# Kernel optimization log

Hardware: AMD Instinct MI355X
Metric: run time of the kernel (lower is better)

## Reference

```python
import jax, jax.numpy as jnp
import numpy as np

NUM_ANCHORS = 32
MAX_DIST = 3
DDE_ROUNDS = 2
DDE_REV_ROUNDS = 2
PE_ANCHOR_DIM = 16


def setup_inputs() -> dict:
    key = jax.random.key(0)
    ks = jax.random.split(key, 20)
    N, Ntext, NT, E, R, D, H = 20000, 19500, 500, 200000, 500, 256, 256
    PE = DDE_ROUNDS + DDE_REV_ROUNDS + PE_ANCHOR_DIM + 3
    s = 0.02
    return {
        "h_ids": jax.random.randint(ks[0], (E,), 0, N),
        "r_ids": jax.random.randint(ks[1], (E,), 0, R),
        "t_ids": jax.random.randint(ks[2], (E,), 0, N),
        "q_emb": jax.random.normal(ks[3], (D,), jnp.float32),
        "entity_embs": jax.random.normal(ks[4], (Ntext, D), jnp.float32),
        "relation_embs": jax.random.normal(ks[5], (R, D), jnp.float32),
        "topic_entity_ids": jax.random.randint(ks[6], (4,), 0, N),
        "num_entities": N,
        "num_non_text_entities": NT,
        "non_text_emb": jax.random.normal(ks[7], (1, D)) * s,
        "dist_emb": jax.random.normal(ks[8], (MAX_DIST + 2, PE_ANCHOR_DIM)) * s,
        "W_enc": jax.random.normal(ks[9], (D + PE, H)) * s,
        "b_enc": jnp.zeros((H,)),
        "gnn_W_msg": jax.random.normal(ks[10], (2, H + D, H)) * s,
        "gnn_W_gate": jax.random.normal(ks[11], (2, 2 * H, H)) * s,
        "gnn_W_upd": jax.random.normal(ks[12], (2, H, H)) * s,
        "W_out": jax.random.normal(ks[13], (H, D)) * s,
        "scorer_W1": jax.random.normal(ks[14], (4 * D + 4, H)) * s,
        "scorer_b1": jnp.zeros((H,)),
        "scorer_W2": jax.random.normal(ks[15], (H, 1)) * s,
        "scorer_b2": jnp.zeros((1,)),
    }


def reference(h_ids, r_ids, t_ids, q_emb, entity_embs, relation_embs,
              topic_entity_ids, num_entities, num_non_text_entities,
              non_text_emb, dist_emb, W_enc, b_enc,
              gnn_W_msg, gnn_W_gate, gnn_W_upd, W_out,
              scorer_W1, scorer_b1, scorer_W2, scorer_b2):
    N = num_entities
    D = q_emb.shape[0]
    E = h_ids.shape[0]
    # assemble all entity embeddings (text + broadcast non-text)
    all_emb = jnp.concatenate(
        [entity_embs, jnp.broadcast_to(non_text_emb, (num_non_text_entities, D))], axis=0)
    # anchor triple selection: question-conditioned triple scores, top-k
    qe = all_emb @ q_emb            # [N]
    qr = relation_embs @ q_emb      # [R]
    tri_score = qe[h_ids] + qr[r_ids] + qe[t_ids]  # [E]
    anchor_scores, anchor_idx = jax.lax.top_k(tri_score, NUM_ANCHORS)
    # topic DDE positional encoding (mean-aggregated label propagation)
    topic = jnp.zeros((N,), all_emb.dtype).at[topic_entity_ids].set(1.0)
    deg_t = jnp.maximum(jnp.zeros((N,)).at[t_ids].add(1.0), 1.0)
    deg_h = jnp.maximum(jnp.zeros((N,)).at[h_ids].add(1.0), 1.0)
    cols = []
    s = topic
    for _ in range(DDE_ROUNDS):
        s = jnp.zeros((N,)).at[t_ids].add(s[h_ids]) / deg_t
        cols.append(s)
    s = topic
    for _ in range(DDE_REV_ROUNDS):
        s = jnp.zeros((N,)).at[h_ids].add(s[t_ids]) / deg_h
        cols.append(s)
    pe_topic = jnp.stack(cols, axis=1)  # [N, 4]
    # anchor proximity PE: bounded BFS distance, embedded
    anchor_mask = (jnp.zeros((N,)).at[h_ids[anchor_idx]].set(1.0)
                   .at[t_ids[anchor_idx]].set(1.0))
    FAR = float(MAX_DIST + 1)
    dist = jnp.where(anchor_mask > 0, 0.0, FAR)
    for _ in range(MAX_DIST):
        c1 = jnp.full((N,), FAR).at[t_ids].min(dist[h_ids] + 1.0)
        c2 = jnp.full((N,), FAR).at[h_ids].min(dist[t_ids] + 1.0)
        dist = jnp.minimum(dist, jnp.minimum(c1, c2))
    pe_anchor = dist_emb[dist.astype(jnp.int32)]  # [N, 16]
    # path indicators (topic flag, anchor-endpoint flag, subgraph mask = full graph)
    path_ind = jnp.stack([topic, anchor_mask, jnp.ones((N,))], axis=1)
    pe_full = jnp.concatenate([pe_topic, pe_anchor, path_ind], axis=1)  # [N, 23]
    # gated GNN refine over the (full) anchor subgraph
    h = jax.nn.relu(jnp.concatenate([all_emb, pe_full], axis=1) @ W_enc + b_enc)
    rel_e = relation_embs[r_ids]  # [E, D]
    for l in range(gnn_W_msg.shape[0]):
        msg = jax.nn.relu(jnp.concatenate([h[h_ids], rel_e], axis=1) @ gnn_W_msg[l])
        agg = jnp.zeros_like(h).at[t_ids].add(msg)
        gate = jax.nn.sigmoid(jnp.concatenate([h, agg], axis=1) @ gnn_W_gate[l])
        h = h + gate * jnp.tanh(agg @ gnn_W_upd[l])
    h_final = h @ W_out  # back to emb_dim, assembled over all entities
    # scalar triple features
    is_anchor = jnp.zeros((E,)).at[anchor_idx].set(1.0)
    a_score = jnp.zeros((E,)).at[anchor_idx].set(jax.lax.stop_gradient(anchor_scores))
    scalar_feats = jnp.stack([is_anchor, a_score, topic[h_ids], topic[t_ids]], axis=1)
    # triple scorer MLP
    feats = jnp.concatenate([
        jnp.broadcast_to(q_emb, (E, D)), h_final[h_ids], rel_e,
        h_final[t_ids], scalar_feats], axis=1)  # [E, 4D+4]
    hid = jax.nn.relu(feats @ scorer_W1 + scorer_b1)
    return (hid @ scorer_W2 + scorer_b2)[:, 0]
```

## Files before the change

### kernel.cpp

```cpp
#include <hip/hip_runtime.h>
#include <math.h>

#define CDIV(a,b) (((a)+(b)-1)/(b))

typedef short short8 __attribute__((ext_vector_type(8)));
typedef float f32x4  __attribute__((ext_vector_type(4)));
typedef unsigned short u16;

__device__ __forceinline__ float warp_sum(float v){
  #pragma unroll
  for (int o=32;o;o>>=1) v += __shfl_down(v,o);
  return v;
}
__device__ __forceinline__ int warp_min(int v){
  #pragma unroll
  for (int o=32;o;o>>=1) v = min(v,__shfl_down(v,o));
  return v;
}
__device__ __forceinline__ u16 f2bf(float f){
  unsigned u = __float_as_uint(f);
  unsigned r = 0x7fffu + ((u>>16)&1u);
  return (u16)((u + r)>>16);
}
__device__ __forceinline__ float bl(u16 v){ return __uint_as_float(((unsigned)v)<<16); }

__global__ __launch_bounds__(256)
void k_rowdot_all(const float* __restrict__ ent, const float* __restrict__ nontext,
                  const float* __restrict__ q, float* __restrict__ qe,
                  int N, int Ntext,
                  const float* __restrict__ rel, float* __restrict__ qr, int R, int nb1){
  int wid = threadIdx.x>>6, lane = threadIdx.x&63;
  const float* src; float* dst; int row;
  if ((int)blockIdx.x < nb1){
    row = blockIdx.x*4 + wid; if (row >= N) return;
    src = (row < Ntext) ? (ent + (size_t)row*256) : nontext;
    dst = qe;
  } else {
    row = (blockIdx.x-nb1)*4 + wid; if (row >= R) return;
    src = rel + (size_t)row*256;
    dst = qr;
  }
  float4 a = *(const float4*)(src + lane*4);
  float4 b = *(const float4*)(q + lane*4);
  float s = a.x*b.x + a.y*b.y + a.z*b.z + a.w*b.w;
  s = warp_sum(s);
  if (!lane) dst[row] = s;
}

__global__ __launch_bounds__(256)
void k_tri(const int* __restrict__ h, const int* __restrict__ r,
           const int* __restrict__ t, const float* __restrict__ qe,
           const float* __restrict__ qr, float* __restrict__ tri,
           float* __restrict__ bmax, int* __restrict__ degh, int* __restrict__ degi, int E){
  __shared__ float red[256];
  int e = blockIdx.x*256 + threadIdx.x;
  float v = -INFINITY;
  if (e < E){
    int hh=h[e], rr=r[e], tt=t[e];
    v = qe[hh] + qr[rr] + qe[tt];
    tri[e] = v;
    atomicAdd(&degh[hh], 1);
    atomicAdd(&degi[tt], 1);
  }
  red[threadIdx.x]=v; __syncthreads();
  for (int s=128;s;s>>=1){ if ((int)threadIdx.x<s) red[threadIdx.x]=fmaxf(red[threadIdx.x],red[threadIdx.x+s]); __syncthreads(); }
  if (!threadIdx.x) bmax[blockIdx.x]=red[0];
}

__global__ __launch_bounds__(64)
void k_thresh(const float* __restrict__ bmax, float* __restrict__ thrT, int nb){
  int lane = threadIdx.x;
  float m = -INFINITY;
  for (int i=lane; i<nb; i+=64) m = fmaxf(m, bmax[i]);
  for (int it=0; it<32; it++){
    float bv = m; int bln = lane;
    #pragma unroll
    for (int o=32;o;o>>=1){
      float ov = __shfl_down(bv,o);
      int   ol = __shfl_down(bln,o);
      if (ov>bv){ bv=ov; bln=ol; }
    }
    float mv = __shfl(bv,0);
    int   wl = __shfl(bln,0);
    if (lane==wl) m = -INFINITY;
    if (it==31 && lane==0) thrT[0]=mv;
  }
}

__global__ void k_compact(const float* __restrict__ tri, const float* __restrict__ thrT,
                          int* __restrict__ cnt, int* __restrict__ ci, float* __restrict__ cv, int E){
  int e = blockIdx.x*256 + threadIdx.x; if (e>=E) return;
  float v = tri[e];
  if (v >= thrT[0]){
    int p = atomicAdd(cnt, 1);
    ci[p]=e; cv[p]=v;
  }
}

__global__ __launch_bounds__(64)
void k_final32(const int* __restrict__ ci, const float* __restrict__ cv, const int* __restrict__ cnt,
               int* __restrict__ ai, float* __restrict__ as,
               const int* __restrict__ h_ids, const int* __restrict__ t_ids,
               const int* __restrict__ topicId, int nTopic,
               float* __restrict__ topic, float* __restrict__ amask){
  int lane = threadIdx.x;
  int C = *cnt; if (C > 1024) C = 1024;
  int nIter = CDIV(C,64);
  unsigned selMask = 0;
  int myai=0; float myas=0.f;
  for (int it=0; it<32; it++){
    float bv=-INFINITY; int bi=0x7fffffff; int bj=-1;
    for (int j=0;j<nIter;j++){
      int p = lane + j*64;
      if (p < C && !((selMask>>j)&1u)){
        float v = cv[p]; int idx = ci[p];
        if (v>bv || (v==bv && idx<bi)){ bv=v; bi=idx; bj=j; }
      }
    }
    int bln = lane;
    #pragma unroll
    for (int o=32;o;o>>=1){
      float ov=__shfl_down(bv,o); int oi=__shfl_down(bi,o);
      int   oj=__shfl_down(bj,o); int ol=__shfl_down(bln,o);
      if (ov>bv || (ov==bv && oi<bi)){ bv=ov; bi=oi; bj=oj; bln=ol; }
    }
    float wv=__shfl(bv,0); int wi=__shfl(bi,0);
    int   wj=__shfl(bj,0); int wl=__shfl(bln,0);
    if (lane==wl) selMask |= (1u<<wj);
    if (lane==it){ myai=wi; myas=wv; }
  }
  if (lane<32){
    ai[lane]=myai; as[lane]=myas;
    int e = myai;
    amask[h_ids[e]]=1.f;
    amask[t_ids[e]]=1.f;
  }
  if (lane<nTopic) topic[topicId[lane]]=1.f;
}

__global__ void k_scan1(const int* __restrict__ degT, const int* __restrict__ degH,
                        int* __restrict__ offsT, int* __restrict__ offsH,
                        int* __restrict__ bsum, int N, int nb){
  __shared__ int s[256];
  int which = (int)blockIdx.x >= nb;
  int b = which ? blockIdx.x - nb : blockIdx.x;
  const int* deg = which ? degH : degT;
  int* offs = which ? offsH : offsT;
  int i = b*256 + threadIdx.x;
  int v = (i<N) ? deg[i] : 0;
  s[threadIdx.x] = v; __syncthreads();
  #pragma unroll
  for (int o=1;o<256;o<<=1){
    int add = (threadIdx.x>=(unsigned)o) ? s[threadIdx.x-o] : 0; __syncthreads();
    s[threadIdx.x] += add; __syncthreads();
  }
  if (i<N) offs[i] = s[threadIdx.x] - v;
  if (threadIdx.x==255) bsum[blockIdx.x] = s[255];
}
__global__ void k_scan2two(int* __restrict__ bsum, int nb){
  __shared__ int s[256];
  int t=threadIdx.x;
  int half = t>>7, idx = t&127;
  int v = (idx<nb)? bsum[half*nb+idx] : 0;
  s[t]=v; __syncthreads();
  #pragma unroll
  for (int o=1;o<128;o<<=1){ int add=(idx>=o)?s[t-o]:0; __syncthreads(); s[t]+=add; __syncthreads(); }
  if (idx<nb) bsum[half*nb+idx] = s[t]-v;
}
__global__ void k_scan3(int* __restrict__ offsT, int* __restrict__ offsH,
                        const int* __restrict__ bsum,
                        int* __restrict__ curT, int* __restrict__ curH, int N, int nb){
  int which = (int)blockIdx.x >= nb;
  int b = which ? blockIdx.x - nb : blockIdx.x;
  int i = b*256+threadIdx.x; if (i>=N) return;
  int* offs = which ? offsH : offsT;
  int* cur  = which ? curH  : curT;
  int o = offs[i] + bsum[blockIdx.x];
  offs[i]=o; cur[i]=o;
}
__global__ void k_place(const int* __restrict__ h, const int* __restrict__ r,
                        const int* __restrict__ t,
                        int* __restrict__ curT, int* __restrict__ curH,
                        int2* __restrict__ ehr, int* __restrict__ eIdx,
                        int* __restrict__ etH, int E){
  int e = blockIdx.x*256+threadIdx.x; if (e>=E) return;
  int hh=h[e], tt=t[e];
  int pos = atomicAdd(&curT[tt], 1);
  ehr[pos] = make_int2(hh, r[e]);
  eIdx[pos] = e;
  int posh = atomicAdd(&curH[hh], 1);
  etH[posh] = tt;
}

__global__ __launch_bounds__(256)
void k_dde2(const int* __restrict__ offsT, const int* __restrict__ degT, const int2* __restrict__ ehr,
            const int* __restrict__ offsH, const int* __restrict__ degH, const int* __restrict__ etH,
            const float* __restrict__ s0, const float* __restrict__ s1,
            float* __restrict__ sn0, float* __restrict__ sn1,
            float* __restrict__ pe4, int c0, int c1,
            const float* __restrict__ amask, int* __restrict__ dist0, int N){
  int wid=threadIdx.x>>6, lane=threadIdx.x&63;
  int i = blockIdx.x*4+wid; if (i>=N) return;
  int dir = blockIdx.y;
  const int* offs = dir ? offsH : offsT;
  const int* deg  = dir ? degH  : degT;
  const float* s  = dir ? s1 : s0;
  float* sn       = dir ? sn1 : sn0;
  int col         = dir ? c1 : c0;
  int start=offs[i], cnt=deg[i];
  float a=0.f;
  if (dir){
    for (int k=lane;k<cnt;k+=64) a += s[etH[start+k]];
  } else {
    for (int k=lane;k<cnt;k+=64) a += s[ehr[start+k].x];
  }
  a = warp_sum(a);
  if (!lane){
    float v = a / fmaxf((float)cnt,1.f);
    if (sn) sn[i]=v;
    pe4[i*4+col]=v;
    if (dist0 && !dir) dist0[i] = (amask[i]>0.f)?0:4;
  }
}

__global__ __launch_bounds__(256)
void k_bfs_g(const int* __restrict__ offsT, const int* __restrict__ degT, const int2* __restrict__ ehr,
             const int* __restrict__ offsH, const int* __restrict__ degH, const int* __restrict__ etH,
             const int* __restrict__ din, int* __restrict__ dout, int N){
  int wid=threadIdx.x>>6, lane=threadIdx.x&63;
  int i = blockIdx.x*4+wid; if (i>=N) return;
  int sT=offsT[i], cT=degT[i];
  int sH=offsH[i], cH=degH[i];
  int best = 4;
  for (int k=lane;k<cT;k+=64) best = min(best, din[ehr[sT+k].x]+1);
  for (int k=lane;k<cH;k+=64) best = min(best, din[etH[sH+k]]+1);
  best = warp_min(best);
  if (!lane) dout[i] = min(din[i], best);
}

__global__ void k_smalls(const float* __restrict__ dist_e, const float* __restrict__ W_enc,
                         float* __restrict__ distW,
                         const float* __restrict__ nontext, float* __restrict__ encnt,
                         const float* __restrict__ q, const float* __restrict__ W1,
                         const float* __restrict__ b1, float* __restrict__ bias2){
  int b = blockIdx.x, j = threadIdx.x;
  if (b < 5){
    const float* Wpe = W_enc + (256+4)*256;
    float s=0.f;
    #pragma unroll
    for (int p=0;p<16;p++) s += dist_e[b*16+p]*Wpe[p*256+j];
    distW[b*256+j]=s;
  } else if (b == 5){
    float s=0.f;
    for (int k=0;k<256;k++) s += nontext[k]*W_enc[k*256+j];
    encnt[j]=s;
  } else {
    float s=b1[j];
    for (int k=0;k<256;k++) s += q[k]*W1[k*256+j];
    bias2[j]=s;
  }
}

__global__ __launch_bounds__(64)
void k_packall(const float* __restrict__ W_enc, const float* __restrict__ W_msg,
               const float* __restrict__ W_gate, const float* __restrict__ W_upd,
               const float* __restrict__ W1, u16* __restrict__ pbAll){
  int f = blockIdx.x, lane = threadIdx.x;
  int tgt, fid, nt16;
  if      (f < 128) { tgt=0; fid=f;      nt16=16; }
  else if (f < 256) { tgt=1; fid=f-128;  nt16=16; }
  else if (f < 384) { tgt=2; fid=f-256;  nt16=16; }
  else if (f < 896) { tgt=3; fid=f-384;  nt16=32; }
  else if (f < 1408){ tgt=4; fid=f-896;  nt16=32; }
  else if (f < 1792){ tgt=5; fid=f-1408; nt16=48; }
  else              { tgt=6; fid=f-1792; nt16=32; }
  int ks = fid/nt16, nt = fid%nt16;
  int kb = ks*32 + 8*(lane>>4);
  int n  = nt*16 + (lane&15);
  u16 v[8];
  #pragma unroll
  for (int i=0;i<8;i++){
    int k = kb+i;
    float x;
    if (tgt==0) x = W_enc[(size_t)k*256+n];
    else if (tgt==1) x = W_msg[(size_t)k*256+n];
    else if (tgt==2) x = W_msg[(size_t)(512+k)*256+n];
    else if (tgt==3 || tgt==4){
      const float* Wg = W_gate + (tgt==4 ? (size_t)512*256 : 0);
      const float* Wu = W_upd  + (tgt==4 ? (size_t)256*256 : 0);
      int blk = n>>4, c = ((blk>>1)<<4) | (n&15);
      if ((blk&1)==0) x = Wg[(size_t)k*256+c];
      else            x = (k<256) ? 0.f : Wu[(size_t)(k-256)*256+c];
    }
    else if (tgt==5){
      if (n<256)      x = W_msg[(size_t)(256+k)*256+n];
      else if (n<512) x = W_msg[(size_t)(768+k)*256+(n-256)];
      else            x = W1[(size_t)(512+k)*256+(n-512)];
    } else {
      if (n<256) x = W1[(size_t)(256+k)*256+n];
      else       x = W1[(size_t)(768+k)*256+(n-256)];
    }
    v[i]=f2bf(x);
  }
  *(uint4*)(pbAll + ((size_t)f*64+lane)*8) = *(uint4*)v;
}

__global__ __launch_bounds__(64)
void k_packf32(const float* __restrict__ W, u16* __restrict__ Bp){
  int f = blockIdx.x, lane = threadIdx.x;
  int ks = f/32, nt = f%32;
  int kb = ks*32 + 8*(lane>>4);
  int n  = nt*16 + (lane&15);
  u16 v[8];
  #pragma unroll
  for (int i=0;i<8;i++) v[i] = f2bf(W[(size_t)(kb+i)*512 + n]);
  *(uint4*)(Bp + ((size_t)f*64+lane)*8) = *(uint4*)v;
}

template<int NCOLS, int CT, int MODE, bool AF32, int MR>
__global__ __launch_bounds__(256)
void k_bgemm(const float* __restrict__ A1f, const u16* __restrict__ A2a,
             const u16* __restrict__ A2b, int K1,
             const u16* __restrict__ Bp, void* __restrict__ Cout,
             const float* __restrict__ xb, const float* __restrict__ W_enc,
             const float* __restrict__ pe4, const int* __restrict__ dist,
             const float* __restrict__ topic, const float* __restrict__ amask,
             const float* __restrict__ distW,
             int M, int K)
{
  constexpr int NT16 = NCOLS/16;
  constexpr int CPB  = NCOLS/CT;
  constexpr int NREP = CPB/32;
  const int tid  = threadIdx.x;
  const int lane = tid & 63;
  const int w    = tid >> 6;
  const int wr   = w >> 1, wc = w & 1;
  const int ct   = blockIdx.y;
  const int row0 = (blockIdx.x*2 + wr)*(16*MR);
  const int lrow = lane & 15;
  const int kc   = lane >> 4;
  int arow[MR];
  #pragma unroll
  for (int m=0;m<MR;m++){
    int rr = row0 + m*16 + lrow;
    arow[m] = (rr >= M) ? M-1 : rr;
  }

  f32x4 acc[MR][NREP];
  #pragma unroll
  for (int m=0;m<MR;m++)
    #pragma unroll
    for (int n=0;n<NREP;n++) acc[m][n] = (f32x4){0.f,0.f,0.f,0.f};

  const int ksteps = K/32;
  const int fcolBase = ct*(CPB/16) + wc*NREP;

  auto do_step = [&](short8* af, int ks){
    const u16* bp = Bp + ((size_t)(ks*NT16 + fcolBase)*64 + lane)*8;
    #pragma unroll
    for (int n=0;n<NREP;n++){
      short8 bf = *(const short8*)(bp + (size_t)n*64*8);
      #pragma unroll
      for (int m=0;m<MR;m++)
        acc[m][n] = __builtin_amdgcn_mfma_f32_16x16x32_bf16(af[m], bf, acc[m][n], 0, 0, 0);
    }
  };

  if (AF32){
    for (int ks=0; ks<ksteps; ks++){
      short8 af[MR];
      #pragma unroll
      for (int m=0;m<MR;m++){
        const float* ap = A1f + (size_t)arow[m]*256 + ks*32 + kc*8;
        float4 a0 = *(const float4*)ap;
        float4 a1 = *(const float4*)(ap+4);
        af[m][0]=(short)f2bf(a0.x); af[m][1]=(short)f2bf(a0.y); af[m][2]=(short)f2bf(a0.z); af[m][3]=(short)f2bf(a0.w);
        af[m][4]=(short)f2bf(a1.x); af[m][5]=(short)f2bf(a1.y); af[m][6]=(short)f2bf(a1.z); af[m][7]=(short)f2bf(a1.w);
      }
      do_step(af, ks);
    }
  } else {
    int s1 = K1>>5; if (s1 > ksteps) s1 = ksteps;
    for (int ks=0; ks<s1; ks++){
      short8 af[MR];
      #pragma unroll
      for (int m=0;m<MR;m++)
        af[m] = *(const short8*)(A2a + (size_t)arow[m]*256 + ks*32 + kc*8);
      do_step(af, ks);
    }
    for (int ks=s1; ks<ksteps; ks++){
      short8 af[MR];
      #pragma unroll
      for (int m=0;m<MR;m++)
        af[m] = *(const short8*)(A2b + (size_t)arow[m]*256 + (ks-s1)*32 + kc*8);
      do_step(af, ks);
    }
  }

  #pragma unroll
  for (int m=0;m<MR;m++){
    #pragma unroll
    for (int r=0;r<4;r++){
      int orow = row0 + m*16 + 4*kc + r;
      if (orow >= M) continue;
      if (MODE==0 || MODE==1){
        #pragma unroll
        for (int n=0;n<NREP;n++){
          int col = ct*CPB + wc*(CPB/2) + n*16 + lrow;
          float v = acc[m][n][r];
          if (MODE==0) ((float*)Cout)[(size_t)orow*NCOLS + col] = v;
          else         ((u16*)Cout)[(size_t)orow*NCOLS + col] = f2bf(v);
        }
      } else if (MODE==5){
        float tp = topic[orow];
        #pragma unroll
        for (int n=0;n<NREP;n++){
          int col = ct*CPB + wc*(CPB/2) + n*16 + lrow;
          float v = acc[m][n][r] + tp*xb[col];
          ((u16*)Cout)[(size_t)orow*NCOLS + col] = f2bf(v);
        }
      } else if (MODE==6){
        #pragma unroll
        for (int n=0;n<NREP;n++){
          int col = ct*CPB + wc*(CPB/2) + n*16 + lrow;
          float v = acc[m][n][r];
          if (col >= 512) v += xb[col-512];
          ((u16*)Cout)[(size_t)orow*NCOLS + col] = f2bf(v);
        }
      } else if (MODE==3){
        float p0=pe4[orow*4+0], p1=pe4[orow*4+1], p2=pe4[orow*4+2], p3=pe4[orow*4+3];
        int dd=dist[orow];
        float tp=topic[orow], am=amask[orow];
        const float* Wpe = W_enc + 256*256;
        #pragma unroll
        for (int n=0;n<NREP;n++){
          int col = ct*CPB + wc*(CPB/2) + n*16 + lrow;
          float v = acc[m][n][r];
          v += xb[col] + Wpe[22*256+col]
             + p0*Wpe[col] + p1*Wpe[256+col] + p2*Wpe[512+col] + p3*Wpe[768+col]
             + distW[dd*256+col] + tp*Wpe[20*256+col] + am*Wpe[21*256+col];
          ((u16*)Cout)[(size_t)orow*256 + col] = f2bf(fmaxf(v, 0.f));
        }
      } else {
        #pragma unroll
        for (int k=0;k<NREP/2;k++){
          int col = (ct*(CPB/32) + wc*(CPB/64) + k)*16 + lrow;
          size_t idx = (size_t)orow*256 + col;
          float g = 1.f/(1.f+expf(-acc[m][2*k][r]));
          float u = tanhf(acc[m][2*k+1][r]);
          float v = bl(A2a[idx]) + g*u;
          ((u16*)Cout)[idx] = f2bf(v);
        }
      }
    }
  }
}

__global__ __launch_bounds__(256)
void k_encnt_fill(const float* __restrict__ encnt, const float* __restrict__ b_enc,
                  const float* __restrict__ W_enc, const float* __restrict__ pe4,
                  const int* __restrict__ dist, const float* __restrict__ topic,
                  const float* __restrict__ amask, const float* __restrict__ distW,
                  u16* __restrict__ hB, int Ntext){
  int i = Ntext + blockIdx.x, j = threadIdx.x;
  const float* Wpe = W_enc + 256*256;
  float p0=pe4[i*4+0], p1=pe4[i*4+1], p2=pe4[i*4+2], p3=pe4[i*4+3];
  int d = dist[i];
  float tp = topic[i], am = amask[i];
  float v = encnt[j] + b_enc[j] + Wpe[22*256+j]
          + p0*Wpe[j] + p1*Wpe[256+j] + p2*Wpe[512+j] + p3*Wpe[768+j]
          + distW[d*256+j] + tp*Wpe[20*256+j] + am*Wpe[21*256+j];
  hB[(size_t)i*256+j] = f2bf(fmaxf(v, 0.f));
}

__global__ __launch_bounds__(256)
void k_agg(const int* __restrict__ offs, const int* __restrict__ degi,
           const int2* __restrict__ ehr,
           const u16* __restrict__ hm, const u16* __restrict__ relC, int colOff,
           u16* __restrict__ agg, int N){
  int wid = threadIdx.x>>6, lane = threadIdx.x&63;
  int i = blockIdx.x*4 + wid; if (i>=N) return;
  int start = offs[i], cnt = degi[i];
  int c4 = lane*4;
  float a0=0.f,a1=0.f,a2=0.f,a3=0.f;
  int k=0;
  for (; k+3<cnt; k+=4){
    int2 hr[4]; uint2 ua[4], ub[4];
    #pragma unroll
    for (int j=0;j<4;j++) hr[j] = ehr[start+k+j];
    #pragma unroll
    for (int j=0;j<4;j++){
      ua[j] = *(const uint2*)(hm + (size_t)hr[j].x*256 + c4);
      ub[j] = *(const uint2*)(relC + (size_t)hr[j].y*768 + colOff + c4);
    }
    #pragma unroll
    for (int j=0;j<4;j++){
      a0 += fmaxf(bl((u16)(ua[j].x&0xffff))+bl((u16)(ub[j].x&0xffff)),0.f);
      a1 += fmaxf(bl((u16)(ua[j].x>>16))  +bl((u16)(ub[j].x>>16)),  0.f);
      a2 += fmaxf(bl((u16)(ua[j].y&0xffff))+bl((u16)(ub[j].y&0xffff)),0.f);
      a3 += fmaxf(bl((u16)(ua[j].y>>16))  +bl((u16)(ub[j].y>>16)),  0.f);
    }
  }
  for (; k<cnt; k++){
    int2 hr = ehr[start+k];
    uint2 ua = *(const uint2*)(hm + (size_t)hr.x*256 + c4);
    uint2 ub = *(const uint2*)(relC + (size_t)hr.y*768 + colOff + c4);
    a0 += fmaxf(bl((u16)(ua.x&0xffff))+bl((u16)(ub.x&0xffff)),0.f);
    a1 += fmaxf(bl((u16)(ua.x>>16))  +bl((u16)(ub.x>>16)),  0.f);
    a2 += fmaxf(bl((u16)(ua.y&0xffff))+bl((u16)(ub.y&0xffff)),0.f);
    a3 += fmaxf(bl((u16)(ua.y>>16))  +bl((u16)(ub.y>>16)),  0.f);
  }
  uint2 o;
  o.x = (unsigned)f2bf(a0) | ((unsigned)f2bf(a1)<<16);
  o.y = (unsigned)f2bf(a2) | ((unsigned)f2bf(a3)<<16);
  *(uint2*)(agg + (size_t)i*256 + c4) = o;
}

__global__ __launch_bounds__(256)
void k_score(const int* __restrict__ offs, const int* __restrict__ degi,
             const int2* __restrict__ ehr, const int* __restrict__ eIdx,
             const u16* __restrict__ UHT, const u16* __restrict__ relC,
             const float* __restrict__ W2,
             const float* __restrict__ b2, float* __restrict__ out, int N){
  int wid = threadIdx.x>>6, lane = threadIdx.x&63;
  int i = blockIdx.x*4 + wid; if (i>=N) return;
  int start = offs[i], cnt = degi[i];
  if (!cnt) return;
  int c = lane*4;
  uint2 ud = *(const uint2*)(UHT + (size_t)i*512 + 256 + c);
  float b0 = bl((u16)(ud.x&0xffff)), b1v = bl((u16)(ud.x>>16));
  float b2v= bl((u16)(ud.y&0xffff)), b3  = bl((u16)(ud.y>>16));
  float4 w = *(const float4*)(W2 + c);
  float bout = b2[0];
  int k=0;
  for (; k+3<cnt; k+=4){
    int2 e[4]; uint2 ua[4], ub[4];
    #pragma unroll
    for (int j=0;j<4;j++) e[j] = ehr[start+k+j];
    #pragma unroll
    for (int j=0;j<4;j++){
      ua[j] = *(const uint2*)(UHT + (size_t)e[j].x*512 + c);
      ub[j] = *(const uint2*)(relC + (size_t)e[j].y*768 + 512 + c);
    }
    float p[4];
    #pragma unroll
    for (int j=0;j<4;j++){
      p[j] = fmaxf(b0 + bl((u16)(ua[j].x&0xffff)) + bl((u16)(ub[j].x&0xffff)),0.f)*w.x
           + fmaxf(b1v+ bl((u16)(ua[j].x>>16))    + bl((u16)(ub[j].x>>16)),  0.f)*w.y
           + fmaxf(b2v+ bl((u16)(ua[j].y&0xffff)) + bl((u16)(ub[j].y&0xffff)),0.f)*w.z
           + fmaxf(b3 + bl((u16)(ua[j].y>>16))    + bl((u16)(ub[j].y>>16)),  0.f)*w.w;
    }
    #pragma unroll
    for (int j=0;j<4;j++) p[j] = warp_sum(p[j]);
    if (!lane){
      #pragma unroll
      for (int j=0;j<4;j++) out[eIdx[start+k+j]] = p[j] + bout;
    }
  }
  for (; k<cnt; k++){
    int2 e0 = ehr[start+k];
    uint2 ua = *(const uint2*)(UHT + (size_t)e0.x*512 + c);
    uint2 ub = *(const uint2*)(relC + (size_t)e0.y*768 + 512 + c);
    float p = fmaxf(b0 + bl((u16)(ua.x&0xffff)) + bl((u16)(ub.x&0xffff)),0.f)*w.x
            + fmaxf(b1v+ bl((u16)(ua.x>>16))    + bl((u16)(ub.x>>16)),  0.f)*w.y
            + fmaxf(b2v+ bl((u16)(ua.y&0xffff)) + bl((u16)(ub.y&0xffff)),0.f)*w.z
            + fmaxf(b3 + bl((u16)(ua.y>>16))    + bl((u16)(ub.y>>16)),  0.f)*w.w;
    p = warp_sum(p);
    if (!lane) out[eIdx[start+k]] = p + bout;
  }
}

__global__ __launch_bounds__(256)
void k_patch(const int* __restrict__ ai, const float* __restrict__ as,
             const int* __restrict__ h_ids, const int* __restrict__ r_ids, const int* __restrict__ t_ids,
             const u16* __restrict__ UHT, const u16* __restrict__ relC,
             const float* __restrict__ W1s, const float* __restrict__ W2,
             const float* __restrict__ b2, float* __restrict__ out){
  int wid = threadIdx.x>>6, lane = threadIdx.x&63;
  int k = blockIdx.x*4 + wid; if (k>=32) return;
  int e = ai[k];
  int h=h_ids[e], r=r_ids[e], t=t_ids[e];
  float aS = as[k];
  int c = lane*4;
  uint2 ua = *(const uint2*)(UHT + (size_t)h*512 + c);
  uint2 ud = *(const uint2*)(UHT + (size_t)t*512 + 256 + c);
  uint2 ub = *(const uint2*)(relC + (size_t)r*768 + 512 + c);
  float4 w0 = *(const float4*)(W1s + 0*256 + c);
  float4 w1 = *(const float4*)(W1s + 1*256 + c);
  float4 acc;
  acc.x = bl((u16)(ua.x&0xffff))+bl((u16)(ub.x&0xffff))+bl((u16)(ud.x&0xffff)) + w0.x + aS*w1.x;
  acc.y = bl((u16)(ua.x>>16))  +bl((u16)(ub.x>>16))  +bl((u16)(ud.x>>16))   + w0.y + aS*w1.y;
  acc.z = bl((u16)(ua.y&0xffff))+bl((u16)(ub.y&0xffff))+bl((u16)(ud.y&0xffff)) + w0.z + aS*w1.z;
  acc.w = bl((u16)(ua.y>>16))  +bl((u16)(ub.y>>16))  +bl((u16)(ud.y>>16))   + w0.w + aS*w1.w;
  acc.x=fmaxf(acc.x,0.f); acc.y=fmaxf(acc.y,0.f); acc.z=fmaxf(acc.z,0.f); acc.w=fmaxf(acc.w,0.f);
  float4 w = *(const float4*)(W2 + c);
  float p = acc.x*w.x + acc.y*w.y + acc.z*w.z + acc.w*w.w;
  p = warp_sum(p);
  if (!lane) out[e] = p + b2[0];
}

extern "C" void kernel_launch(void* const* d_in, const int* in_sizes, int n_in,
                              void* d_out, int out_size, void* d_ws, size_t ws_size,
                              hipStream_t stream)
{
  const int*   h_ids   = (const int*)d_in[0];
  const int*   r_ids   = (const int*)d_in[1];
  const int*   t_ids   = (const int*)d_in[2];
  const float* q       = (const float*)d_in[3];
  const float* ent     = (const float*)d_in[4];
  const float* rel     = (const float*)d_in[5];
  const int*   topicId = (const int*)d_in[6];
  const float* nontext = (const float*)d_in[9];
  const float* dist_e  = (const float*)d_in[10];
  const float* W_enc   = (const float*)d_in[11];
  const float* b_enc   = (const float*)d_in[12];
  const float* W_msg   = (const float*)d_in[13];
  const float* W_gate  = (const float*)d_in[14];
  const float* W_upd   = (const float*)d_in[15];
  const float* W_out   = (const float*)d_in[16];
  const float* W1      = (const float*)d_in[17];
  const float* b1      = (const float*)d_in[18];
  const float* W2      = (const float*)d_in[19];
  const float* b2      = (const float*)d_in[20];
  float* out = (float*)d_out;

  const int E = in_sizes[0];
  const int Ntext = in_sizes[4]/256;
  const int R = in_sizes[5]/256;
  const int NT = 500;
  const int N = Ntext + NT;
  const int nTopic = in_sizes[6];
  const int BIGK1 = 1<<28;

  char* ws = (char*)d_ws;
  size_t off = 0;
  auto alloc = [&](size_t bytes)->void*{
    size_t o = (off + 255) & ~(size_t)255;
    off = o + bytes;
    return (void*)(ws + o);
  };
  u16*   hB1   = (u16*)  alloc((size_t)N*256*2);
  u16*   hB2   = (u16*)  alloc((size_t)N*256*2);
  u16*   hmB   = (u16*)  alloc((size_t)N*256*2);
  u16*   aggB  = (u16*)  alloc((size_t)N*256*2);
  u16*   relC  = (u16*)  alloc((size_t)R*768*2);
  u16*   UHT   = (u16*)  alloc((size_t)N*512*2);
  float* WcombF= (float*)alloc((size_t)256*512*4);
  u16*   pbWcomb=(u16*)  alloc((size_t)256*512*2);
  float* qe    = (float*)alloc((size_t)N*4);
  float* qr    = (float*)alloc((size_t)R*4);
  float* tri   = (float*)alloc((size_t)E*4);
  float* bmax  = (float*)alloc(1024*4);
  float* thrT  = (float*)alloc(4);
  int*   ci    = (int*)  alloc((size_t)E*4);
  float* cv    = (float*)alloc((size_t)E*4);
  int*   ai    = (int*)  alloc(32*4);
  float* as    = (float*)alloc(32*4);
  float* pe4   = (float*)alloc((size_t)N*16);
  int*   dA    = (int*)  alloc((size_t)N*4);
  int*   dB    = (int*)  alloc((size_t)N*4);
  float* distW = (float*)alloc(5*256*4);
  float* encnt = (float*)alloc(256*4);
  float* bias2 = (float*)alloc(256*4);
  int*   offsT = (int*)  alloc((size_t)N*4);
  int*   offsH = (int*)  alloc((size_t)N*4);
  int*   bsum  = (int*)  alloc(256*4);
  int*   curT  = (int*)  alloc((size_t)N*4);
  int*   curH  = (int*)  alloc((size_t)N*4);
  int2*  ehr   = (int2*) alloc((size_t)E*8);
  int*   eIdx  = (int*)  alloc((size_t)E*4);
  int*   etH   = (int*)  alloc((size_t)E*4);
  float* sA    = (float*)alloc((size_t)N*4);
  float* sB    = (float*)alloc((size_t)N*4);
  u16*   pbAll = (u16*)  alloc((size_t)2048*512*2);
  int*   cnt   = (int*)  alloc(4);
  float* topic = (float*)alloc((size_t)N*4);
  float* amask = (float*)alloc((size_t)N*4);
  int*   deghI = (int*)  alloc((size_t)N*4);
  int*   degiI = (int*)  alloc((size_t)N*4);
  (void)ws_size; (void)n_in; (void)out_size;

  size_t zbytes = (char*)(degiI + N) - (char*)cnt;
  hipMemsetAsync(cnt, 0, zbytes, stream);

  u16* pbWenc = pbAll + (size_t)0*512;
  u16* pbWmT0 = pbAll + (size_t)128*512;
  u16* pbWmT1 = pbAll + (size_t)256*512;
  u16* pbGU0  = pbAll + (size_t)384*512;
  u16* pbGU1  = pbAll + (size_t)896*512;
  u16* pbRelC = pbAll + (size_t)1408*512;
  u16* pbW1ht = pbAll + (size_t)1792*512;

  const float* tW = W1 + (size_t)(1024+2)*256;

  k_packall<<<2048,64,0,stream>>>(W_enc, W_msg, W_gate, W_upd, W1, pbAll);
  k_bgemm<512,8,0,true,1><<<dim3(8,8),256,0,stream>>>(W_out, nullptr, nullptr, BIGK1, pbW1ht, WcombF,
      nullptr,nullptr,nullptr,nullptr,nullptr,nullptr,nullptr, 256, 256);
  k_packf32<<<256,64,0,stream>>>(WcombF, pbWcomb);

  int nb1 = CDIV(N,4);
  k_rowdot_all<<<nb1+CDIV(R,4),256,0,stream>>>(ent, nontext, q, qe, N, Ntext, rel, qr, R, nb1);
  int nbE = CDIV(E,256);
  k_tri<<<nbE,256,0,stream>>>(h_ids, r_ids, t_ids, qe, qr, tri, bmax, deghI, degiI, E);
  k_thresh<<<1,64,0,stream>>>(bmax, thrT, nbE);
  k_compact<<<nbE,256,0,stream>>>(tri, thrT, cnt, ci, cv, E);
  k_final32<<<1,64,0,stream>>>(ci, cv, cnt, ai, as, h_ids, t_ids, topicId, nTopic, topic, amask);

  int nb = CDIV(N,256);
  k_scan1<<<2*nb,256,0,stream>>>(degiI, deghI, offsT, offsH, bsum, N, nb);
  k_scan2two<<<1,256,0,stream>>>(bsum, nb);
  k_scan3<<<2*nb,256,0,stream>>>(offsT, offsH, bsum, curT, curH, N, nb);
  k_place<<<nbE,256,0,stream>>>(h_ids, r_ids, t_ids, curT, curH, ehr, eIdx, etH, E);

  int nbN4 = CDIV(N,4);
  k_dde2<<<dim3(nbN4,2),256,0,stream>>>(offsT, degiI, ehr, offsH, deghI, etH,
      topic, topic, sB, sA, pe4, 0, 2, nullptr, nullptr, N);
  k_dde2<<<dim3(nbN4,2),256,0,stream>>>(offsT, degiI, ehr, offsH, deghI, etH,
      sB, sA, nullptr, nullptr, pe4, 1, 3, amask, dA, N);

  k_bfs_g<<<nbN4,256,0,stream>>>(offsT, degiI, ehr, offsH, deghI, etH, dA, dB, N);
  k_bfs_g<<<nbN4,256,0,stream>>>(offsT, degiI, ehr, offsH, deghI, etH, dB, dA, N);
  k_bfs_g<<<nbN4,256,0,stream>>>(offsT, degiI, ehr, offsH, deghI, etH, dA, dB, N);

  k_smalls<<<7,256,0,stream>>>(dist_e, W_enc, distW, nontext, encnt, q, W1, b1, bias2);

  k_bgemm<768,6,6,true,1><<<dim3(CDIV(R,32),6),256,0,stream>>>(rel, nullptr, nullptr, BIGK1, pbRelC, relC,
      bias2,nullptr,nullptr,nullptr,nullptr,nullptr,nullptr, R, 256);

  k_bgemm<256,2,3,true,2><<<dim3(CDIV(Ntext,64),2),256,0,stream>>>(ent, nullptr, nullptr, BIGK1, pbWenc, hB1,
      b_enc, W_enc, pe4, dB, topic, amask, distW, Ntext, 256);
  k_encnt_fill<<<N-Ntext,256,0,stream>>>(encnt, b_enc, W_enc, pe4, dB, topic, amask, distW, hB1, Ntext);

  for (int l=0;l<2;l++){
    const u16* pT = l ? pbWmT1 : pbWmT0;
    const u16* pGU = l ? pbGU1 : pbGU0;
    u16* hinB  = l ? hB2 : hB1;
    u16* houtB = l ? hB1 : hB2;
    k_bgemm<256,2,1,false,2><<<dim3(CDIV(N,64),2),256,0,stream>>>(nullptr, hinB, nullptr, BIGK1, pT, hmB,
        nullptr,nullptr,nullptr,nullptr,nullptr,nullptr,nullptr, N, 256);
    k_agg<<<CDIV(N,4),256,0,stream>>>(offsT, degiI, ehr, hmB, relC, l*256, aggB, N);
    k_bgemm<512,2,4,false,2><<<dim3(CDIV(N,64),2),256,0,stream>>>(nullptr, hinB, aggB, 256, pGU, houtB,
        nullptr,nullptr,nullptr,nullptr,nullptr,nullptr,nullptr, N, 512);
  }

  k_bgemm<512,2,5,false,2><<<dim3(CDIV(N,64),2),256,0,stream>>>(nullptr, hB1, nullptr, BIGK1, pbWcomb, UHT,
      tW,nullptr,nullptr,nullptr,topic,nullptr,nullptr, N, 256);

  k_score<<<CDIV(N,4),256,0,stream>>>(offsT, degiI, ehr, eIdx, UHT, relC, W2, b2, out, N);
  k_patch<<<8,256,0,stream>>>(ai, as, h_ids, r_ids, t_ids, UHT, relC,
                              W1+(size_t)1024*256, W2, b2, out);
}
```

Measured before the change: 384.2 us.

## Fuse small setup kernels, BFS steps, and non-text encoder rows into existing launches

Merges the distW/bias2 small GEMVs into the weight-pack kernel and moves the distance initialisation into the scan and place kernels. Two BFS steps now run as a third grid slice of the DDE kernels, since they are independent of DDE. Non-text entity rows are handled inside the encoder GEMM by reading a shared alternate row, which removes the separate fill kernel. The aim is fewer kernel launches and less serialisation on the stream, at the cost of more branching and heavier per-thread work in the merged small GEMV blocks.

```diff
diff --git a/kernel.cpp b/kernel.cpp
--- a/kernel.cpp
+++ b/kernel.cpp
@@ -169,7 +169,8 @@
 }
 __global__ void k_scan3(int* __restrict__ offsT, int* __restrict__ offsH,
                         const int* __restrict__ bsum,
-                        int* __restrict__ curT, int* __restrict__ curH, int N, int nb){
+                        int* __restrict__ curT, int* __restrict__ curH,
+                        int* __restrict__ dinit, int N, int nb){
   int which = (int)blockIdx.x >= nb;
   int b = which ? blockIdx.x - nb : blockIdx.x;
   int i = b*256+threadIdx.x; if (i>=N) return;
@@ -177,12 +178,14 @@
   int* cur  = which ? curH  : curT;
   int o = offs[i] + bsum[blockIdx.x];
   offs[i]=o; cur[i]=o;
+  if (!which) dinit[i] = 4;
 }
 __global__ void k_place(const int* __restrict__ h, const int* __restrict__ r,
                         const int* __restrict__ t,
                         int* __restrict__ curT, int* __restrict__ curH,
                         int2* __restrict__ ehr, int* __restrict__ eIdx,
-                        int* __restrict__ etH, int E){
+                        int* __restrict__ etH,
+                        const int* __restrict__ ai, int* __restrict__ dA, int E){
   int e = blockIdx.x*256+threadIdx.x; if (e>=E) return;
   int hh=h[e], tt=t[e];
   int pos = atomicAdd(&curT[tt], 1);
@@ -190,18 +193,34 @@
   eIdx[pos] = e;
   int posh = atomicAdd(&curH[hh], 1);
   etH[posh] = tt;
+  if (e < 32){
+    int ae = ai[e];
+    dA[h[ae]] = 0;
+    dA[t[ae]] = 0;
+  }
 }
 
 __global__ __launch_bounds__(256)
-void k_dde2(const int* __restrict__ offsT, const int* __restrict__ degT, const int2* __restrict__ ehr,
-            const int* __restrict__ offsH, const int* __restrict__ degH, const int* __restrict__ etH,
-            const float* __restrict__ s0, const float* __restrict__ s1,
-            float* __restrict__ sn0, float* __restrict__ sn1,
-            float* __restrict__ pe4, int c0, int c1,
-            const float* __restrict__ amask, int* __restrict__ dist0, int N){
+void k_dbx(const int* __restrict__ offsT, const int* __restrict__ degT, const int2* __restrict__ ehr,
+           const int* __restrict__ offsH, const int* __restrict__ degH, const int* __restrict__ etH,
+           const float* __restrict__ s0, const float* __restrict__ s1,
+           float* __restrict__ sn0, float* __restrict__ sn1,
+           float* __restrict__ pe4, int c0, int c1,
+           const int* __restrict__ din, int* __restrict__ dout, int N){
   int wid=threadIdx.x>>6, lane=threadIdx.x&63;
   int i = blockIdx.x*4+wid; if (i>=N) return;
-  int dir = blockIdx.y;
+  int ph = blockIdx.y;
+  if (ph == 2){
+    int sT=offsT[i], cT=degT[i];
+    int sH=offsH[i], cH=degH[i];
+    int best = 4;
+    for (int k=lane;k<cT;k+=64) best = min(best, din[ehr[sT+k].x]+1);
+    for (int k=lane;k<cH;k+=64) best = min(best, din[etH[sH+k]]+1);
+    best = warp_min(best);
+    if (!lane) dout[i] = min(din[i], best);
+    return;
+  }
+  int dir = ph;
   const int* offs = dir ? offsH : offsT;
   const int* deg  = dir ? degH  : degT;
   const float* s  = dir ? s1 : s0;
@@ -219,7 +238,6 @@
     float v = a / fmaxf((float)cnt,1.f);
     if (sn) sn[i]=v;
     pe4[i*4+col]=v;
-    if (dist0 && !dir) dist0[i] = (amask[i]>0.f)?0:4;
   }
 }
 
@@ -238,34 +256,37 @@
   if (!lane) dout[i] = min(din[i], best);
 }
 
-__global__ void k_smalls(const float* __restrict__ dist_e, const float* __restrict__ W_enc,
-                         float* __restrict__ distW,
-                         const float* __restrict__ nontext, float* __restrict__ encnt,
-                         const float* __restrict__ q, const float* __restrict__ W1,
-                         const float* __restrict__ b1, float* __restrict__ bias2){
-  int b = blockIdx.x, j = threadIdx.x;
-  if (b < 5){
-    const float* Wpe = W_enc + (256+4)*256;
-    float s=0.f;
-    #pragma unroll
-    for (int p=0;p<16;p++) s += dist_e[b*16+p]*Wpe[p*256+j];
-    distW[b*256+j]=s;
-  } else if (b == 5){
-    float s=0.f;
-    for (int k=0;k<256;k++) s += nontext[k]*W_enc[k*256+j];
-    encnt[j]=s;
-  } else {
-    float s=b1[j];
-    for (int k=0;k<256;k++) s += q[k]*W1[k*256+j];
-    bias2[j]=s;
-  }
-}
-
 __global__ __launch_bounds__(64)
 void k_packall(const float* __restrict__ W_enc, const float* __restrict__ W_msg,
                const float* __restrict__ W_gate, const float* __restrict__ W_upd,
-               const float* __restrict__ W1, u16* __restrict__ pbAll){
+               const float* __restrict__ W1, u16* __restrict__ pbAll,
+               const float* __restrict__ dist_e, float* __restrict__ distW,
+               const float* __restrict__ q, const float* __restrict__ b1,
+               float* __restrict__ bias2){
   int f = blockIdx.x, lane = threadIdx.x;
+  if (f >= 2048){
+    int b = f - 2048;
+    if (b < 5){
+      const float* Wpe = W_enc + (256+4)*256;
+      #pragma unroll
+      for (int jj=0;jj<4;jj++){
+        int j = lane + jj*64;
+        float s=0.f;
+        #pragma unroll
+        for (int p=0;p<16;p++) s += dist_e[b*16+p]*Wpe[p*256+j];
+        distW[b*256+j]=s;
+      }
+    } else {
+      #pragma unroll
+      for (int jj=0;jj<4;jj++){
+        int j = lane + jj*64;
+        float s=b1[j];
+        for (int k=0;k<256;k++) s += q[k]*W1[k*256+j];
+        bias2[j]=s;
+      }
+    }
+    return;
+  }
   int tgt, fid, nt16;
   if      (f < 128) { tgt=0; fid=f;      nt16=16; }
   else if (f < 256) { tgt=1; fid=f-128;  nt16=16; }
@@ -319,8 +340,8 @@
 
 template<int NCOLS, int CT, int MODE, bool AF32, int MR>
 __global__ __launch_bounds__(256)
-void k_bgemm(const float* __restrict__ A1f, const u16* __restrict__ A2a,
-             const u16* __restrict__ A2b, int K1,
+void k_bgemm(const float* __restrict__ A1f, const float* __restrict__ A1alt,
+             const u16* __restrict__ A2a, const u16* __restrict__ A2b, int K1,
              const u16* __restrict__ Bp, void* __restrict__ Cout,
              const float* __restrict__ xb, const float* __restrict__ W_enc,
              const float* __restrict__ pe4, const int* __restrict__ dist,
@@ -371,7 +392,8 @@
       short8 af[MR];
       #pragma unroll
       for (int m=0;m<MR;m++){
-        const float* ap = A1f + (size_t)arow[m]*256 + ks*32 + kc*8;
+        const float* ap = (arow[m] < K1) ? (A1f + (size_t)arow[m]*256 + ks*32 + kc*8)
+                                         : (A1alt + ks*32 + kc*8);
         float4 a0 = *(const float4*)ap;
         float4 a1 = *(const float4*)(ap+4);
         af[m][0]=(short)f2bf(a0.x); af[m][1]=(short)f2bf(a0.y); af[m][2]=(short)f2bf(a0.z); af[m][3]=(short)f2bf(a0.w);
@@ -457,23 +479,6 @@
 }
 
 __global__ __launch_bounds__(256)
-void k_encnt_fill(const float* __restrict__ encnt, const float* __restrict__ b_enc,
-                  const float* __restrict__ W_enc, const float* __restrict__ pe4,
-                  const int* __restrict__ dist, const float* __restrict__ topic,
-                  const float* __restrict__ amask, const float* __restrict__ distW,
-                  u16* __restrict__ hB, int Ntext){
-  int i = Ntext + blockIdx.x, j = threadIdx.x;
-  const float* Wpe = W_enc + 256*256;
-  float p0=pe4[i*4+0], p1=pe4[i*4+1], p2=pe4[i*4+2], p3=pe4[i*4+3];
-  int d = dist[i];
-  float tp = topic[i], am = amask[i];
-  float v = encnt[j] + b_enc[j] + Wpe[22*256+j]
-          + p0*Wpe[j] + p1*Wpe[256+j] + p2*Wpe[512+j] + p3*Wpe[768+j]
-          + distW[d*256+j] + tp*Wpe[20*256+j] + am*Wpe[21*256+j];
-  hB[(size_t)i*256+j] = f2bf(fmaxf(v, 0.f));
-}
-
-__global__ __launch_bounds__(256)
 void k_agg(const int* __restrict__ offs, const int* __restrict__ degi,
            const int2* __restrict__ ehr,
            const u16* __restrict__ hm, const u16* __restrict__ relC, int colOff,
@@ -660,7 +665,6 @@
   int*   dA    = (int*)  alloc((size_t)N*4);
   int*   dB    = (int*)  alloc((size_t)N*4);
   float* distW = (float*)alloc(5*256*4);
-  float* encnt = (float*)alloc(256*4);
   float* bias2 = (float*)alloc(256*4);
   int*   offsT = (int*)  alloc((size_t)N*4);
   int*   offsH = (int*)  alloc((size_t)N*4);
@@ -693,8 +697,9 @@
 
   const float* tW = W1 + (size_t)(1024+2)*256;
 
-  k_packall<<<2048,64,0,stream>>>(W_enc, W_msg, W_gate, W_upd, W1, pbAll);
-  k_bgemm<512,8,0,true,1><<<dim3(8,8),256,0,stream>>>(W_out, nullptr, nullptr, BIGK1, pbW1ht, WcombF,
+  k_packall<<<2054,64,0,stream>>>(W_enc, W_msg, W_gate, W_upd, W1, pbAll,
+                                  dist_e, distW, q, b1, bias2);
+  k_bgemm<512,8,0,true,1><<<dim3(8,8),256,0,stream>>>(W_out, nullptr, nullptr, nullptr, BIGK1, pbW1ht, WcombF,
       nullptr,nullptr,nullptr,nullptr,nullptr,nullptr,nullptr, 256, 256);
   k_packf32<<<256,64,0,stream>>>(WcombF, pbWcomb);
 
@@ -709,41 +714,35 @@
   int nb = CDIV(N,256);
   k_scan1<<<2*nb,256,0,stream>>>(degiI, deghI, offsT, offsH, bsum, N, nb);
   k_scan2two<<<1,256,0,stream>>>(bsum, nb);
-  k_scan3<<<2*nb,256,0,stream>>>(offsT, offsH, bsum, curT, curH, N, nb);
-  k_place<<<nbE,256,0,stream>>>(h_ids, r_ids, t_ids, curT, curH, ehr, eIdx, etH, E);
+  k_scan3<<<2*nb,256,0,stream>>>(offsT, offsH, bsum, curT, curH, dA, N, nb);
+  k_place<<<nbE,256,0,stream>>>(h_ids, r_ids, t_ids, curT, curH, ehr, eIdx, etH, ai, dA, E);
 
   int nbN4 = CDIV(N,4);
-  k_dde2<<<dim3(nbN4,2),256,0,stream>>>(offsT, degiI, ehr, offsH, deghI, etH,
-      topic, topic, sB, sA, pe4, 0, 2, nullptr, nullptr, N);
-  k_dde2<<<dim3(nbN4,2),256,0,stream>>>(offsT, degiI, ehr, offsH, deghI, etH,
-      sB, sA, nullptr, nullptr, pe4, 1, 3, amask, dA, N);
-
+  k_dbx<<<dim3(nbN4,3),256,0,stream>>>(offsT, degiI, ehr, offsH, deghI, etH,
+      topic, topic, sB, sA, pe4, 0, 2, dA, dB, N);
+  k_dbx<<<dim3(nbN4,3),256,0,stream>>>(offsT, degiI, ehr, offsH, deghI, etH,
+      sB, sA, nullptr, nullptr, pe4, 1, 3, dB, dA, N);
   k_bfs_g<<<nbN4,256,0,stream>>>(offsT, degiI, ehr, offsH, deghI, etH, dA, dB, N);
-  k_bfs_g<<<nbN4,256,0,stream>>>(offsT, degiI, ehr, offsH, deghI, etH, dB, dA, N);
-  k_bfs_g<<<nbN4,256,0,stream>>>(offsT, degiI, ehr, offsH, deghI, etH, dA, dB, N);
-
-  k_smalls<<<7,256,0,stream>>>(dist_e, W_enc, distW, nontext, encnt, q, W1, b1, bias2);
-
-  k_bgemm<768,6,6,true,1><<<dim3(CDIV(R,32),6),256,0,stream>>>(rel, nullptr, nullptr, BIGK1, pbRelC, relC,
+
+  k_bgemm<768,6,6,true,1><<<dim3(CDIV(R,32),6),256,0,stream>>>(rel, nullptr, nullptr, nullptr, BIGK1, pbRelC, relC,
       bias2,nullptr,nullptr,nullptr,nullptr,nullptr,nullptr, R, 256);
 
-  k_bgemm<256,2,3,true,2><<<dim3(CDIV(Ntext,64),2),256,0,stream>>>(ent, nullptr, nullptr, BIGK1, pbWenc, hB1,
-      b_enc, W_enc, pe4, dB, topic, amask, distW, Ntext, 256);
-  k_encnt_fill<<<N-Ntext,256,0,stream>>>(encnt, b_enc, W_enc, pe4, dB, topic, amask, distW, hB1, Ntext);
+  k_bgemm<256,2,3,true,2><<<dim3(CDIV(N,64),2),256,0,stream>>>(ent, nontext, nullptr, nullptr, Ntext, pbWenc, hB1,
+      b_enc, W_enc, pe4, dB, topic, amask, distW, N, 256);
 
   for (int l=0;l<2;l++){
     const u16* pT = l ? pbWmT1 : pbWmT0;
     const u16* pGU = l ? pbGU1 : pbGU0;
     u16* hinB  = l ? hB2 : hB1;
     u16* houtB = l ? hB1 : hB2;
-    k_bgemm<256,2,1,false,2><<<dim3(CDIV(N,64),2),256,0,stream>>>(nullptr, hinB, nullptr, BIGK1, pT, hmB,
+    k_bgemm<256,2,1,false,2><<<dim3(CDIV(N,64),2),256,0,stream>>>(nullptr, nullptr, hinB, nullptr, BIGK1, pT, hmB,
         nullptr,nullptr,nullptr,nullptr,nullptr,nullptr,nullptr, N, 256);
     k_agg<<<CDIV(N,4),256,0,stream>>>(offsT, degiI, ehr, hmB, relC, l*256, aggB, N);
-    k_bgemm<512,2,4,false,2><<<dim3(CDIV(N,64),2),256,0,stream>>>(nullptr, hinB, aggB, 256, pGU, houtB,
+    k_bgemm<512,2,4,false,2><<<dim3(CDIV(N,64),2),256,0,stream>>>(nullptr, nullptr, hinB, aggB, 256, pGU, houtB,
         nullptr,nullptr,nullptr,nullptr,nullptr,nullptr,nullptr, N, 512);
   }
 
-  k_bgemm<512,2,5,false,2><<<dim3(CDIV(N,64),2),256,0,stream>>>(nullptr, hB1, nullptr, BIGK1, pbWcomb, UHT,
+  k_bgemm<512,2,5,false,2><<<dim3(CDIV(N,64),2),256,0,stream>>>(nullptr, nullptr, hB1, nullptr, BIGK1, pbWcomb, UHT,
       tW,nullptr,nullptr,nullptr,topic,nullptr,nullptr, N, 256);
 
   k_score<<<CDIV(N,4),256,0,stream>>>(offsT, degiI, ehr, eIdx, UHT, relC, W2, b2, out, N);
```

Result: no change. 390.1 us (+1.5%).
